# Kernel tuning notes

Measured on AMD Instinct MI355X. Metric: run time of the kernel, lower is better.

## Reference

```python
import jax, jax.numpy as jnp
import numpy as np

EPS = 1e-5
BS, NA, NC, NL, NPTS, ED, NG = 1, 900, 6, 4, 13, 256, 8
GD = ED // NG
IMG_W, IMG_H = 704.0, 256.0
FMAP_HW = [(64, 176), (32, 88), (16, 44), (8, 22)]


def _ln(x, g, b):
    m = x.mean(-1, keepdims=True)
    v = ((x - m) ** 2).mean(-1, keepdims=True)
    return (x - m) / jnp.sqrt(v + EPS) * g + b


def _grid_sample(img, grid):
    # img: [N,C,H,W]; grid: [N,P,Q,2] in [-1,1]; bilinear, zeros padding, align_corners=False
    N, C, H, W = img.shape
    gx = jnp.clip((grid[..., 0] + 1.0) * (W * 0.5) - 0.5, -1e4, 1e4)
    gy = jnp.clip((grid[..., 1] + 1.0) * (H * 0.5) - 0.5, -1e4, 1e4)
    x0 = jnp.floor(gx); y0 = jnp.floor(gy)
    wx1 = gx - x0; wy1 = gy - y0; wx0 = 1.0 - wx1; wy0 = 1.0 - wy1
    x0i = x0.astype(jnp.int32); y0i = y0.astype(jnp.int32)
    flat = img.reshape(N, C, H * W)

    def corner(xi, yi, wgt):
        valid = (xi >= 0) & (xi < W) & (yi >= 0) & (yi < H)
        idx = (jnp.clip(yi, 0, H - 1) * W + jnp.clip(xi, 0, W - 1))
        g = jax.vmap(lambda f, i: f[:, i])(flat, idx.reshape(N, -1))  # [N,C,P*Q]
        g = g.reshape(N, C, idx.shape[1], idx.shape[2])
        return g * (wgt * valid)[:, None]

    return (corner(x0i, y0i, wx0 * wy0) + corner(x0i + 1, y0i, wx1 * wy0)
            + corner(x0i, y0i + 1, wx0 * wy1) + corner(x0i + 1, y0i + 1, wx1 * wy1))


def setup_inputs() -> dict:
    key = jax.random.key(0)
    ks = jax.random.split(key, 20)
    d = {}
    d['instance_feature'] = jax.random.normal(ks[0], (BS, NA, ED), jnp.float32)
    xyz = jax.random.normal(ks[1], (BS, NA, 3), jnp.float32) * 1.5
    size = jax.random.normal(ks[2], (BS, NA, 3), jnp.float32) * 0.3
    theta = jax.random.uniform(ks[3], (BS, NA, 1), jnp.float32) * (2.0 * np.pi)
    vel = jax.random.normal(ks[4], (BS, NA, 3), jnp.float32) * 0.1
    d['anchor'] = jnp.concatenate([xyz, size, jnp.sin(theta), jnp.cos(theta), vel], -1)
    d['anchor_embed'] = jax.random.normal(ks[5], (BS, NA, ED), jnp.float32)
    for i, (h, w) in enumerate(FMAP_HW):
        d[f'fmap{i}'] = jax.random.normal(ks[6 + i], (BS, NC, ED, h, w), jnp.float32)
    base = jnp.array([[80., 0., 0., 352.], [0., 80., 0., 128.],
                      [0., 0., 0., 1.], [0., 0., 0., 1.]], jnp.float32)
    proj = jnp.tile(base, (BS, NC, 1, 1))
    proj = proj.at[:, :, :2, :].add(jax.random.normal(ks[10], (BS, NC, 2, 4), jnp.float32) * 2.0)
    d['projection_mat'] = proj
    d['image_wh'] = jnp.broadcast_to(jnp.array([IMG_W, IMG_H], jnp.float32), (BS, NC, 2))
    d['fix_scale'] = jnp.array([[0, 0, 0], [0.45, 0, 0], [-0.45, 0, 0], [0, 0.45, 0],
                                [0, -0.45, 0], [0, 0, 0.45], [0, 0, -0.45]], jnp.float32)

    def w(k, shape):
        return jax.random.normal(k, shape, jnp.float32) * 0.02

    d['lfc_w'] = w(ks[11], (ED, 6 * 3)); d['lfc_b'] = jnp.zeros((18,), jnp.float32)
    d['cam_w1'] = w(ks[12], (12, ED)); d['cam_b1'] = jnp.zeros((ED,), jnp.float32)
    d['cam_g1'] = jnp.ones((ED,), jnp.float32); d['cam_be1'] = jnp.zeros((ED,), jnp.float32)
    d['cam_w2'] = w(ks[13], (ED, ED)); d['cam_b2'] = jnp.zeros((ED,), jnp.float32)
    d['cam_g2'] = jnp.ones((ED,), jnp.float32); d['cam_be2'] = jnp.zeros((ED,), jnp.float32)
    d['wfc_w'] = w(ks[14], (ED, NG * NL * NPTS)); d['wfc_b'] = jnp.zeros((NG * NL * NPTS,), jnp.float32)
    d['op_w'] = w(ks[15], (ED, ED)); d['op_b'] = jnp.zeros((ED,), jnp.float32)
    return d


def reference(instance_feature, anchor, anchor_embed, fmap0, fmap1, fmap2, fmap3,
              projection_mat, image_wh, fix_scale, lfc_w, lfc_b,
              cam_w1, cam_b1, cam_g1, cam_be1, cam_w2, cam_b2, cam_g2, cam_be2,
              wfc_w, wfc_b, op_w, op_b):
    bs, na = instance_feature.shape[:2]
    # ---- keypoint generation ----
    size = jnp.exp(anchor[..., None, 3:6])                       # [bs,na,1,3]
    kp = fix_scale * size                                        # [bs,na,7,3]
    ls = jax.nn.sigmoid(instance_feature @ lfc_w + lfc_b).reshape(bs, na, -1, 3) - 0.5
    kp = jnp.concatenate([kp, ls * size], axis=-2)               # [bs,na,NPTS,3]
    sin, cos = anchor[..., 6:7], anchor[..., 7:8]                # [bs,na,1]
    kx, ky, kz = kp[..., 0], kp[..., 1], kp[..., 2]
    key_points = jnp.stack([cos * kx - sin * ky, sin * kx + cos * ky, kz], -1) \
                 + anchor[..., None, 0:3]                        # [bs,na,NPTS,3]
    # ---- per-cam/level/point group weights ----
    feat = instance_feature + anchor_embed
    cam_in = projection_mat[:, :, :3].reshape(bs, NC, 12)
    h = jax.nn.relu(cam_in @ cam_w1 + cam_b1); h = _ln(h, cam_g1, cam_be1)
    h = jax.nn.relu(h @ cam_w2 + cam_b2); cam_embed = _ln(h, cam_g2, cam_be2)
    f = feat[:, :, None] + cam_embed[:, None]                    # [bs,na,NC,ED]
    wts = (f @ wfc_w + wfc_b).reshape(bs, na, NC * NL * NPTS, NG)
    wts = jax.nn.softmax(wts, axis=-2).reshape(bs, na, NC, NL, NPTS, NG)
    # ---- multi-cam projection + bilinear sampling ----
    pts = jnp.concatenate([key_points, jnp.ones_like(key_points[..., :1])], -1)
    p2d = jnp.einsum('bcij,banj->bcani', projection_mat, pts)    # [bs,NC,na,NPTS,4]
    p2d = p2d[..., :2] / jnp.maximum(p2d[..., 2:3], 1e-5)
    p2d = p2d / image_wh[:, :, None, None]
    grid = (p2d * 2.0 - 1.0).reshape(bs * NC, na, NPTS, 2)
    feats = jnp.stack([_grid_sample(fm.reshape(bs * NC, ED, fm.shape[-2], fm.shape[-1]), grid)
                       for fm in (fmap0, fmap1, fmap2, fmap3)], axis=1)  # [bs*NC,NL,ED,na,NPTS]
    feats = feats.reshape(bs, NC, NL, ED, na, NPTS).transpose(0, 4, 1, 2, 5, 3)  # [bs,na,NC,NL,NPTS,ED]
    # ---- group-weighted fusion over cams & levels, then sum over points ----
    fg = feats.reshape(bs, na, NC, NL, NPTS, NG, GD)
    fused = jnp.einsum('bnclpg,bnclpgd->bnpgd', wts, fg).reshape(bs, na, NPTS, ED)
    fused = fused.sum(axis=2)                                    # [bs,na,ED]
    out = fused @ op_w + op_b
    return jnp.concatenate([out, instance_feature], axis=-1)     # [bs,na,2*ED]
```

## Files before the change

kernel.cpp:

```cpp
#include <hip/hip_runtime.h>
#include <stdint.h>

#define NA 900
#define NC 6
#define NL 4
#define NPTS 13
#define ED 256
#define NG 8
#define LNEPS 1e-5f
#define NTRANS 1416
#define NCOPY 672
#define NSAMP 312
#define LGS 313

struct PIn { const void* p[24]; };

__device__ __forceinline__ float b2f(unsigned short u){
  union { uint32_t i; float f; } v; v.i = ((uint32_t)u)<<16; return v.f;
}
__device__ __forceinline__ unsigned short f2b(float f){
  union { float f; uint32_t i; } v; v.f = f;
  uint32_t r = v.i + 0x7FFFu + ((v.i>>16)&1u);
  return (unsigned short)(r>>16);
}
#define BLO(u) __uint_as_float((u)<<16)
#define BHI(u) __uint_as_float((u)&0xffff0000u)

__device__ __forceinline__ float ldx(const void* p, int i, bool bf){
  return bf ? b2f(((const unsigned short*)p)[i]) : ((const float*)p)[i];
}

__device__ __forceinline__ bool sniff_bf(const unsigned short* __restrict__ u16){
  int lane = threadIdx.x & 63;
  unsigned short u = u16[2*lane];
  int e = (u>>7)&0xFF;
  int sane = (e>=110 && e<=135) ? 1 : 0;
  #pragma unroll
  for (int m=32;m;m>>=1) sane += __shfl_xor(sane, m);
  return sane >= 48;
}

__device__ __forceinline__ void blockReduce2(float& a, float& b, float* lds){
  #pragma unroll
  for (int m=32;m;m>>=1){ a += __shfl_xor(a,m); b += __shfl_xor(b,m); }
  int w = threadIdx.x>>6;
  if ((threadIdx.x&63)==0){ lds[w]=a; lds[w+4]=b; }
  __syncthreads();
  a = lds[0]+lds[1]+lds[2]+lds[3];
  b = lds[4]+lds[5]+lds[6]+lds[7];
  __syncthreads();
}

__global__ __launch_bounds__(256) void k_init(PIn in,
                                              unsigned short* __restrict__ wfcw_h,
                                              unsigned short* __restrict__ opw_h,
                                              float* __restrict__ Bc){
  const bool bf = sniff_bf((const unsigned short*)in.p[0]);
  const int tid = threadIdx.x;
  int b = blockIdx.x;

  __shared__ float h[ED];
  __shared__ float cE[ED];
  __shared__ float red8[8];
  __shared__ float part[4][64];

  if (b < NCOPY){
    int idx = b*256 + tid;
    if (idx < 106496){
      wfcw_h[idx] = bf ? ((const unsigned short*)in.p[20])[idx]
                       : f2b(((const float*)in.p[20])[idx]);
    } else {
      int j = idx - 106496;
      opw_h[j] = bf ? ((const unsigned short*)in.p[22])[j]
                    : f2b(((const float*)in.p[22])[j]);
    }
    return;
  }
  b -= NCOPY;
  {
    const void* proj = in.p[7];
    const void* w1 = in.p[12]; const void* b1 = in.p[13];
    const void* g1 = in.p[14]; const void* be1 = in.p[15];
    const void* w2 = in.p[16]; const void* b2 = in.p[17];
    const void* g2 = in.p[18]; const void* be2 = in.p[19];
    const void* wfcw = in.p[20]; const void* wfcb = in.p[21];
    const int c = b/7, colt = b - (b/7)*7;
    float ci[12];
    #pragma unroll
    for (int i=0;i<12;i++) ci[i] = ldx(proj, c*16+i, bf);
    float acc = ldx(b1, tid, bf);
    #pragma unroll
    for (int k=0;k<12;k++) acc += ci[k]*ldx(w1, k*ED+tid, bf);
    float x = fmaxf(acc, 0.f);
    float s=x, q=x*x;
    blockReduce2(s,q,red8);
    float mean = s*(1.f/ED), var = q*(1.f/ED)-mean*mean;
    h[tid] = (x-mean)*rsqrtf(var+LNEPS)*ldx(g1,tid,bf) + ldx(be1,tid,bf);
    __syncthreads();
    acc = ldx(b2, tid, bf);
    #pragma unroll 8
    for (int k=0;k<ED;k++) acc += h[k]*ldx(w2, k*ED+tid, bf);
    x = fmaxf(acc,0.f);
    s=x; q=x*x;
    blockReduce2(s,q,red8);
    mean = s*(1.f/ED); var = q*(1.f/ED)-mean*mean;
    cE[tid] = (x-mean)*rsqrtf(var+LNEPS)*ldx(g2,tid,bf) + ldx(be2,tid,bf);
    __syncthreads();
    const int kc = tid>>6, colL = tid&63, col = colt*64+colL;
    float a = 0.f;
    if (col < 416){
      #pragma unroll 8
      for (int k=0;k<64;k++) a += cE[kc*64+k]*ldx(wfcw, (kc*64+k)*416+col, bf);
    }
    part[kc][colL] = a;
    __syncthreads();
    if (kc==0 && col<416)
      Bc[c*416+col] = part[0][colL]+part[1][colL]+part[2][colL]+part[3][colL] + ldx(wfcb,col,bf);
  }
}

__global__ __launch_bounds__(256) void k_work(PIn in,
                                              unsigned short* __restrict__ tf,
                                              const unsigned short* __restrict__ wfcw_h,
                                              const float* __restrict__ Bc,
                                              uint4* __restrict__ gdesc, int* __restrict__ mcnt,
                                              void* __restrict__ outv){
  const bool bf = sniff_bf((const unsigned short*)in.p[0]);
  const int tid = threadIdx.x;
  int b = blockIdx.x;

  __shared__ unsigned short TT[2][64][64];
  __shared__ float ifs[ED];
  __shared__ float fe[ED];
  __shared__ float lg2[8*LGS];
  __shared__ float kp[13][3];
  __shared__ float sc[8];
  __shared__ float lsv[18];
  __shared__ int scnt;

  if (b < NTRANS){
    const int tiles[4] = {44,11,3,1};
    const int HWs[4]   = {11264,2816,704,176};
    const int TFO[4]   = {0,17301504,21626880,22708224};
    int l, local;
    if      (b < 1056){ l=0; local=b;      }
    else if (b < 1320){ l=1; local=b-1056; }
    else if (b < 1392){ l=2; local=b-1320; }
    else              { l=3; local=b-1392; }
    int pt = local % tiles[l]; int rest = local / tiles[l];
    int ct = rest & 3; int c = rest >> 2;
    const int HW = HWs[l];
    const int px0 = pt*256;
    const void* src = in.p[3+l];
    const int j8 = tid & 7;
    const int w8 = tid >> 3;

    uint4 v[2][4];
    float4 cf[2][4][2];
    if (bf){
      #pragma unroll
      for (int p=0;p<2;p++){
        int ch = ct*64 + p*32 + w8;
        size_t rowb = (size_t)(c*ED+ch)*HW;
        #pragma unroll
        for (int q=0;q<4;q++){
          int pxs = px0 + q*64 + j8*8;
          v[p][q] = (pxs < HW)
            ? *reinterpret_cast<const uint4*>((const unsigned short*)src + rowb + pxs)
            : make_uint4(0,0,0,0);
        }
      }
    } else {
      #pragma unroll
      for (int p=0;p<2;p++){
        int ch = ct*64 + p*32 + w8;
        size_t rowb = (size_t)(c*ED+ch)*HW;
        #pragma unroll
        for (int q=0;q<4;q++){
          int pxs = px0 + q*64 + j8*8;
          if (pxs < HW){
            cf[p][q][0] = *reinterpret_cast<const float4*>((const float*)src + rowb + pxs);
            cf[p][q][1] = *reinterpret_cast<const float4*>((const float*)src + rowb + pxs + 4);
          } else {
            cf[p][q][0] = make_float4(0.f,0.f,0.f,0.f);
            cf[p][q][1] = cf[p][q][0];
          }
        }
      }
    }
    for (int q=0;q<4;q++){
      if (px0 + q*64 >= HW) break;
      uint4 wv[2];
      if (bf){
        wv[0] = v[0][q]; wv[1] = v[1][q];
      } else {
        #pragma unroll
        for (int p=0;p<2;p++){
          wv[p].x = (uint32_t)f2b(cf[p][q][0].x) | ((uint32_t)f2b(cf[p][q][0].y)<<16);
          wv[p].y = (uint32_t)f2b(cf[p][q][0].z) | ((uint32_t)f2b(cf[p][q][0].w)<<16);
          wv[p].z = (uint32_t)f2b(cf[p][q][1].x) | ((uint32_t)f2b(cf[p][q][1].y)<<16);
          wv[p].w = (uint32_t)f2b(cf[p][q][1].z) | ((uint32_t)f2b(cf[p][q][1].w)<<16);
        }
      }
      const int buf = q & 1;
      #pragma unroll
      for (int p=0;p<2;p++){
        int r = p*32 + w8;
        int g8 = (j8 ^ (r>>3))<<3;
        *reinterpret_cast<uint4*>(&TT[buf][r][g8]) = wv[p];
      }
      __syncthreads();
      #pragma unroll
      for (int p=0;p<2;p++){
        int pxl = p*32 + w8;
        int px  = px0 + q*64 + pxl;
        int colq = (((pxl>>3) ^ j8)<<3) | (pxl & 7);
        int rb = j8*8;
        unsigned short t0 = TT[buf][rb+0][colq], t1 = TT[buf][rb+1][colq];
        unsigned short t2 = TT[buf][rb+2][colq], t3 = TT[buf][rb+3][colq];
        unsigned short t4 = TT[buf][rb+4][colq], t5 = TT[buf][rb+5][colq];
        unsigned short t6 = TT[buf][rb+6][colq], t7 = TT[buf][rb+7][colq];
        uint4 o;
        o.x = (uint32_t)t0 | ((uint32_t)t1<<16);
        o.y = (uint32_t)t2 | ((uint32_t)t3<<16);
        o.z = (uint32_t)t4 | ((uint32_t)t5<<16);
        o.w = (uint32_t)t6 | ((uint32_t)t7<<16);
        if (px < HW)
          *reinterpret_cast<uint4*>(tf + TFO[l] + (size_t)c*HW*ED + (size_t)px*ED + ct*64 + j8*8) = o;
      }
    }
    return;
  }
  const int n = b - NTRANS;
  const void* p_inst = in.p[0];
  const void* p_anc  = in.p[1];
  const void* p_ae   = in.p[2];
  const void* p_proj = in.p[7];
  const void* p_imwh = in.p[8];
  const void* p_fixs = in.p[9];
  const void* p_lw   = in.p[10];
  const void* p_lb   = in.p[11];

  {
    if (tid==0) scnt = 0;
    float iv = ldx(p_inst, n*ED+tid, bf);
    ifs[tid] = iv;
    fe[tid]  = iv + ldx(p_ae, n*ED+tid, bf);
    if (bf) ((unsigned short*)outv)[n*512+256+tid] = f2b(iv);
    else    ((float*)outv)[n*512+256+tid]          = iv;
    if (tid >= 256-8){
      int t = tid - (256-8);
      if (t < 3)       sc[t] = ldx(p_anc, n*11+t, bf);
      else if (t == 3) sc[3] = ldx(p_anc, n*11+6, bf);
      else if (t == 4) sc[4] = ldx(p_anc, n*11+7, bf);
      else             sc[t] = __expf(ldx(p_anc, n*11+t-2, bf));
    }
  }
  __syncthreads();
  if (tid < 144){
    int d = tid>>3, j = tid&7;
    float a = 0.f;
    #pragma unroll 8
    for (int k=j*32;k<j*32+32;k++) a += ifs[k]*ldx(p_lw, k*18+d, bf);
    a += __shfl_xor(a,1); a += __shfl_xor(a,2); a += __shfl_xor(a,4);
    if (j==0){
      a += ldx(p_lb, d, bf);
      lsv[d] = 1.f/(1.f+__expf(-a)) - 0.5f;
    }
  }
  __syncthreads();
  if (tid < 13){
    float kx,ky,kz;
    if (tid < 7){
      kx = ldx(p_fixs, tid*3+0, bf)*sc[5];
      ky = ldx(p_fixs, tid*3+1, bf)*sc[6];
      kz = ldx(p_fixs, tid*3+2, bf)*sc[7];
    } else {
      int j = tid-7;
      kx = lsv[j*3+0]*sc[5]; ky = lsv[j*3+1]*sc[6]; kz = lsv[j*3+2]*sc[7];
    }
    kp[tid][0] = sc[4]*kx - sc[3]*ky + sc[0];
    kp[tid][1] = sc[3]*kx + sc[4]*ky + sc[1];
    kp[tid][2] = kz + sc[2];
  }
  {
    int col2 = (tid < 160) ? tid+256 : 415;
    float a0 = 0.f, a1 = 0.f;
    #pragma unroll 4
    for (int k=0;k<ED;k++){
      float fv = fe[k];
      a0 += fv*b2f(wfcw_h[k*416+tid]);
      a1 += fv*b2f(wfcw_h[k*416+col2]);
    }
    const int g = tid & 7, rr = tid >> 3;
    const int g2 = col2 & 7, rr2 = col2 >> 3;
    #pragma unroll
    for (int c=0;c<NC;c++){
      lg2[g*LGS + c*52 + rr] = a0 + Bc[c*416+tid];
      if (tid < 160) lg2[g2*LGS + c*52 + rr2] = a1 + Bc[c*416+col2];
    }
  }
  __syncthreads();
  {
    const int g = tid>>5, j = tid&31;
    float v[10]; float mx = -1e30f;
    #pragma unroll
    for (int i=0;i<10;i++){
      int e = j + 32*i;
      float val = -1e30f;
      if (e < NSAMP){ val = lg2[g*LGS + e]; mx = fmaxf(mx, val); }
      v[i] = val;
    }
    #pragma unroll
    for (int mk=16;mk;mk>>=1) mx = fmaxf(mx, __shfl_xor(mx, mk, 32));
    float sum = 0.f;
    #pragma unroll
    for (int i=0;i<10;i++){
      if (j + 32*i < NSAMP){ float ex = __expf(v[i]-mx); v[i] = ex; sum += ex; }
    }
    #pragma unroll
    for (int mk=16;mk;mk>>=1) sum += __shfl_xor(sum, mk, 32);
    float inv = 1.f/sum;
    #pragma unroll
    for (int i=0;i<10;i++){
      int e = j + 32*i;
      if (e < NSAMP) lg2[g*LGS + e] = v[i]*inv;
    }
  }
  __syncthreads();
  #pragma unroll
  for (int pass=0;pass<2;pass++){
    int s = tid + pass*256;
    if (s < NSAMP){
      int c = s/52, rr = s - c*52;
      int l = rr/13, p = rr - l*13;
      float m[12];
      #pragma unroll
      for (int i=0;i<12;i++) m[i] = ldx(p_proj, c*16+i, bf);
      float X=kp[p][0], Y=kp[p][1], Z=kp[p][2];
      float x = m[0]*X + m[1]*Y + m[2]*Z  + m[3];
      float y = m[4]*X + m[5]*Y + m[6]*Z  + m[7];
      float z = m[8]*X + m[9]*Y + m[10]*Z + m[11];
      float d = fmaxf(z, 1e-5f);
      float px = x/(d*ldx(p_imwh, c*2+0, bf)), py = y/(d*ldx(p_imwh, c*2+1, bf));
      const int W = 176>>l, H = 64>>l;
      const int TFO[4] = {0,17301504,21626880,22708224};
      float gx = fminf(fmaxf(px*(float)W - 0.5f, -10000.f), 10000.f);
      float gy = fminf(fmaxf(py*(float)H - 0.5f, -10000.f), 10000.f);
      float xf = floorf(gx), yf = floorf(gy);
      int x0 = (int)xf, y0 = (int)yf;
      float wx1 = gx-xf, wy1 = gy-yf;
      float wx0 = 1.f-wx1, wy0 = 1.f-wy1;
      bool vx0 = (x0>=0)&&(x0<W),   vx1 = (x0+1>=0)&&(x0+1<W);
      bool vy0 = (y0>=0)&&(y0<H),   vy1 = (y0+1>=0)&&(y0+1<H);
      float w00 = (vx0&&vy0) ? wx0*wy0 : 0.f;
      float w10 = (vx1&&vy0) ? wx1*wy0 : 0.f;
      float w01 = (vx0&&vy1) ? wx0*wy1 : 0.f;
      float w11 = (vx1&&vy1) ? wx1*wy1 : 0.f;
      if (w00+w10+w01+w11 != 0.f){
        int cx0 = min(max(x0,0),W-1), cx1 = min(max(x0+1,0),W-1);
        int cy0 = min(max(y0,0),H-1), cy1 = min(max(y0+1,0),H-1);
        uint32_t cam = (uint32_t)TFO[l] + (uint32_t)(c*H*W)*ED;
        uint4 bi, wv;
        bi.x = cam + (uint32_t)(cy0*W+cx0)*ED;
        bi.y = cam + (uint32_t)(cy0*W+cx1)*ED;
        bi.z = cam + (uint32_t)(cy1*W+cx0)*ED;
        bi.w = cam + (uint32_t)(cy1*W+cx1)*ED;
        wv.x = __float_as_uint(w00); wv.y = __float_as_uint(w10);
        wv.z = __float_as_uint(w01); wv.w = __float_as_uint(w11);
        float4 wa = make_float4(lg2[0*LGS+s], lg2[1*LGS+s], lg2[2*LGS+s], lg2[3*LGS+s]);
        float4 wb = make_float4(lg2[4*LGS+s], lg2[5*LGS+s], lg2[6*LGS+s], lg2[7*LGS+s]);
        int slot = atomicAdd(&scnt, 1);
        uint4* dst = gdesc + (size_t)(n*NSAMP + slot)*4;
        dst[0] = bi;
        dst[1] = wv;
        dst[2] = *reinterpret_cast<uint4*>(&wa);
        dst[3] = *reinterpret_cast<uint4*>(&wb);
      }
    }
  }
  __syncthreads();
  if (tid==0) mcnt[n] = scnt;
}

__global__ __launch_bounds__(512, 4) void k_gather(
    const unsigned short* __restrict__ tf,
    const unsigned short* __restrict__ opw_h, const uint4* __restrict__ gdesc,
    const int* __restrict__ mcnt, const void* __restrict__ rawinst,
    const void* __restrict__ opb, void* __restrict__ outv){
  const int n = blockIdx.x, tid = threadIdx.x;
  const bool bf = sniff_bf((const unsigned short*)rawinst);

  __shared__ uint4 ldesc[NSAMP*4];
  __shared__ float red[8][ED+4];
  __shared__ float fu[ED];

  const int m = mcnt[n];
  {
    const uint4* src = gdesc + (size_t)n*NSAMP*4;
    for (int j=tid; j < m*4; j += 512) ldesc[j] = src[j];
  }
  __syncthreads();

  {
    const int strm = tid>>5, lane32 = tid&31;
    const int ch8 = lane32*8, gg = lane32>>2;
    float acc[8] = {0,0,0,0,0,0,0,0};
    int i = strm;
    for (; i + 16 < m; i += 32){
      uint4 biA = ldesc[i*4],      wfA = ldesc[i*4+1];
      uint4 biB = ldesc[(i+16)*4], wfB = ldesc[(i+16)*4+1];
      float wgA = reinterpret_cast<const float*>(&ldesc[i*4+2])[gg];
      float wgB = reinterpret_cast<const float*>(&ldesc[(i+16)*4+2])[gg];
      uint4 a00 = *reinterpret_cast<const uint4*>(tf + biA.x + ch8);
      uint4 a10 = *reinterpret_cast<const uint4*>(tf + biA.y + ch8);
      uint4 a01 = *reinterpret_cast<const uint4*>(tf + biA.z + ch8);
      uint4 a11 = *reinterpret_cast<const uint4*>(tf + biA.w + ch8);
      uint4 b00 = *reinterpret_cast<const uint4*>(tf + biB.x + ch8);
      uint4 b10 = *reinterpret_cast<const uint4*>(tf + biB.y + ch8);
      uint4 b01 = *reinterpret_cast<const uint4*>(tf + biB.z + ch8);
      uint4 b11 = *reinterpret_cast<const uint4*>(tf + biB.w + ch8);
      float pA00 = wgA*__uint_as_float(wfA.x), pA10 = wgA*__uint_as_float(wfA.y);
      float pA01 = wgA*__uint_as_float(wfA.z), pA11 = wgA*__uint_as_float(wfA.w);
      float pB00 = wgB*__uint_as_float(wfB.x), pB10 = wgB*__uint_as_float(wfB.y);
      float pB01 = wgB*__uint_as_float(wfB.z), pB11 = wgB*__uint_as_float(wfB.w);
      acc[0] += pA00*BLO(a00.x)+pA10*BLO(a10.x)+pA01*BLO(a01.x)+pA11*BLO(a11.x)
              + pB00*BLO(b00.x)+pB10*BLO(b10.x)+pB01*BLO(b01.x)+pB11*BLO(b11.x);
      acc[1] += pA00*BHI(a00.x)+pA10*BHI(a10.x)+pA01*BHI(a01.x)+pA11*BHI(a11.x)
              + pB00*BHI(b00.x)+pB10*BHI(b10.x)+pB01*BHI(b01.x)+pB11*BHI(b11.x);
      acc[2] += pA00*BLO(a00.y)+pA10*BLO(a10.y)+pA01*BLO(a01.y)+pA11*BLO(a11.y)
              + pB00*BLO(b00.y)+pB10*BLO(b10.y)+pB01*BLO(b01.y)+pB11*BLO(b11.y);
      acc[3] += pA00*BHI(a00.y)+pA10*BHI(a10.y)+pA01*BHI(a01.y)+pA11*BHI(a11.y)
              + pB00*BHI(b00.y)+pB10*BHI(b10.y)+pB01*BHI(b01.y)+pB11*BHI(b11.y);
      acc[4] += pA00*BLO(a00.z)+pA10*BLO(a10.z)+pA01*BLO(a01.z)+pA11*BLO(a11.z)
              + pB00*BLO(b00.z)+pB10*BLO(b10.z)+pB01*BLO(b01.z)+pB11*BLO(b11.z);
      acc[5] += pA00*BHI(a00.z)+pA10*BHI(a10.z)+pA01*BHI(a01.z)+pA11*BHI(a11.z)
              + pB00*BHI(b00.z)+pB10*BHI(b10.z)+pB01*BHI(b01.z)+pB11*BHI(b11.z);
      acc[6] += pA00*BLO(a00.w)+pA10*BLO(a10.w)+pA01*BLO(a01.w)+pA11*BLO(a11.w)
              + pB00*BLO(b00.w)+pB10*BLO(b10.w)+pB01*BLO(b01.w)+pB11*BLO(b11.w);
      acc[7] += pA00*BHI(a00.w)+pA10*BHI(a10.w)+pA01*BHI(a01.w)+pA11*BHI(a11.w)
              + pB00*BHI(b00.w)+pB10*BHI(b10.w)+pB01*BHI(b01.w)+pB11*BHI(b11.w);
    }
    for (; i < m; i += 16){
      uint4 bi = ldesc[i*4], wf = ldesc[i*4+1];
      float wg = reinterpret_cast<const float*>(&ldesc[i*4+2])[gg];
      uint4 q00 = *reinterpret_cast<const uint4*>(tf + bi.x + ch8);
      uint4 q10 = *reinterpret_cast<const uint4*>(tf + bi.y + ch8);
      uint4 q01 = *reinterpret_cast<const uint4*>(tf + bi.z + ch8);
      uint4 q11 = *reinterpret_cast<const uint4*>(tf + bi.w + ch8);
      float p00 = wg*__uint_as_float(wf.x), p10 = wg*__uint_as_float(wf.y);
      float p01 = wg*__uint_as_float(wf.z), p11 = wg*__uint_as_float(wf.w);
      acc[0] += p00*BLO(q00.x)+p10*BLO(q10.x)+p01*BLO(q01.x)+p11*BLO(q11.x);
      acc[1] += p00*BHI(q00.x)+p10*BHI(q10.x)+p01*BHI(q01.x)+p11*BHI(q11.x);
      acc[2] += p00*BLO(q00.y)+p10*BLO(q10.y)+p01*BLO(q01.y)+p11*BLO(q11.y);
      acc[3] += p00*BHI(q00.y)+p10*BHI(q10.y)+p01*BHI(q01.y)+p11*BHI(q11.y);
      acc[4] += p00*BLO(q00.z)+p10*BLO(q10.z)+p01*BLO(q01.z)+p11*BLO(q11.z);
      acc[5] += p00*BHI(q00.z)+p10*BHI(q10.z)+p01*BHI(q01.z)+p11*BHI(q11.z);
      acc[6] += p00*BLO(q00.w)+p10*BLO(q10.w)+p01*BLO(q01.w)+p11*BLO(q11.w);
      acc[7] += p00*BHI(q00.w)+p10*BHI(q10.w)+p01*BHI(q01.w)+p11*BHI(q11.w);
    }
    #pragma unroll
    for (int j=0;j<8;j++) acc[j] += __shfl_xor(acc[j], 32);
    const int w = tid>>6;
    if ((tid&63) < 32){
      *reinterpret_cast<float4*>(&red[w][ch8])   = make_float4(acc[0],acc[1],acc[2],acc[3]);
      *reinterpret_cast<float4*>(&red[w][ch8+4]) = make_float4(acc[4],acc[5],acc[6],acc[7]);
    }
  }
  __syncthreads();
  if (tid < 256){
    float r = 0.f;
    #pragma unroll
    for (int i=0;i<8;i++) r += red[i][tid];
    fu[tid] = r;
  }
  __syncthreads();
  {
    const int col = tid & 255, half = tid >> 8;
    const int k0 = half*128;
    float a = 0.f;
    #pragma unroll 8
    for (int k=k0;k<k0+128;k++) a += fu[k]*b2f(opw_h[k*ED+col]);
    red[half][col] = a;
  }
  __syncthreads();
  if (tid < 256){
    float v = ldx(opb, tid, bf) + red[0][tid] + red[1][tid];
    if (bf) ((unsigned short*)outv)[n*512+tid] = f2b(v);
    else    ((float*)outv)[n*512+tid]          = v;
  }
}

extern "C" void kernel_launch(void* const* d_in, const int* in_sizes, int n_in,
                              void* d_out, int out_size, void* d_ws, size_t ws_size,
                              hipStream_t stream){
  char* ws = (char*)d_ws;
  size_t off = 0;
  auto alloc = [&](size_t bytes)->char*{
    char* p = ws + off; off += (bytes + 63) & ~size_t(63); return p;
  };
  unsigned short* tf = (unsigned short*)alloc((size_t)22978560*2);
  unsigned short* wfcw_h = (unsigned short*)alloc((size_t)106496*2);
  unsigned short* opw_h  = (unsigned short*)alloc((size_t)65536*2);
  float* Bc     = (float*)alloc((size_t)NC*416*4);
  uint4* gdesc  = (uint4*)alloc((size_t)NA*NSAMP*64);
  int*   mcnt   = (int*)alloc((size_t)NA*4);

  PIn in;
  for (int i=0;i<24;i++) in.p[i] = d_in[i];

  k_init<<<NCOPY + 42, 256, 0, stream>>>(in, wfcw_h, opw_h, Bc);
  k_work<<<NTRANS + NA, 256, 0, stream>>>(in, tf, wfcw_h, Bc, gdesc, mcnt, d_out);
  k_gather<<<NA, 512, 0, stream>>>(tf, opw_h, gdesc, mcnt, d_in[0], d_in[23], d_out);
}
```

Before: 260.9 us.

## Stream fp32 feature-map transpose tiles via async global-to-LDS double buffering

```diff
diff --git a/kernel.cpp b/kernel.cpp
--- a/kernel.cpp
+++ b/kernel.cpp
@@ -28,6 +28,12 @@
 
 __device__ __forceinline__ float ldx(const void* p, int i, bool bf){
   return bf ? b2f(((const unsigned short*)p)[i]) : ((const float*)p)[i];
+}
+
+__device__ __forceinline__ void gload_lds16(const void* g, void* l){
+  __builtin_amdgcn_global_load_lds(
+      (const __attribute__((address_space(1))) void*)g,
+      (__attribute__((address_space(3))) void*)l, 16, 0, 0);
 }
 
 __device__ __forceinline__ bool sniff_bf(const unsigned short* __restrict__ u16){
@@ -129,14 +135,7 @@
   const int tid = threadIdx.x;
   int b = blockIdx.x;
 
-  __shared__ unsigned short TT[2][64][64];
-  __shared__ float ifs[ED];
-  __shared__ float fe[ED];
-  __shared__ float lg2[8*LGS];
-  __shared__ float kp[13][3];
-  __shared__ float sc[8];
-  __shared__ float lsv[18];
-  __shared__ int scnt;
+  __shared__ __align__(16) char smem[32768];
 
   if (b < NTRANS){
     const int tiles[4] = {44,11,3,1};
@@ -155,9 +154,66 @@
     const int j8 = tid & 7;
     const int w8 = tid >> 3;
 
-    uint4 v[2][4];
-    float4 cf[2][4][2];
-    if (bf){
+    int nq = 4;
+    while (nq > 1 && px0 + (nq-1)*64 >= HW) nq--;
+
+    if (!bf){
+      float* TTf = (float*)smem;
+      const int wv = tid >> 6;
+      const int ln = tid & 63;
+      const int rq = ln >> 4;
+      const int g  = ln & 15;
+
+      auto issueph = [&](int q){
+        const int pxq = px0 + q*64;
+        float* dst0 = TTf + (q&1)*4096;
+        #pragma unroll
+        for (int i=0;i<4;i++){
+          int r   = wv*16 + i*4 + rq;
+          int swz = (r>>3) & 7;
+          int px  = pxq + 4*(g ^ swz);
+          if (px + 4 > HW) px = HW - 4;
+          const float* gsrc = (const float*)src + (size_t)(c*ED + ct*64 + r)*HW + px;
+          gload_lds16(gsrc, (void*)(dst0 + (wv*16 + i*4)*64));
+        }
+      };
+
+      issueph(0);
+      for (int q=0; q<nq; q++){
+        if (q+1 < nq){
+          issueph(q+1);
+          asm volatile("s_waitcnt vmcnt(4)" ::: "memory");
+        } else {
+          asm volatile("s_waitcnt vmcnt(0)" ::: "memory");
+        }
+        __builtin_amdgcn_s_barrier();
+        const float* T = TTf + (q&1)*4096;
+        #pragma unroll
+        for (int p=0;p<2;p++){
+          int pxl = p*32 + w8;
+          int px  = px0 + q*64 + pxl;
+          int s   = 4*((pxl>>2) ^ j8) + (pxl&3);
+          if (px < HW){
+            unsigned short u[8];
+            #pragma unroll
+            for (int k=0;k<8;k++)
+              u[k] = f2b(T[(j8*8+k)*64 + s]);
+            uint4 o;
+            o.x = (uint32_t)u[0] | ((uint32_t)u[1]<<16);
+            o.y = (uint32_t)u[2] | ((uint32_t)u[3]<<16);
+            o.z = (uint32_t)u[4] | ((uint32_t)u[5]<<16);
+            o.w = (uint32_t)u[6] | ((uint32_t)u[7]<<16);
+            *reinterpret_cast<uint4*>(tf + TFO[l] + (size_t)c*HW*ED + (size_t)px*ED + ct*64 + j8*8) = o;
+          }
+        }
+        __builtin_amdgcn_s_barrier();
+      }
+      return;
+    }
+    {
+      typedef unsigned short u16tile[64][64];
+      u16tile* TT = (u16tile*)smem;
+      uint4 v[2][4];
       #pragma unroll
       for (int p=0;p<2;p++){
         int ch = ct*64 + p*32 + w8;
@@ -170,68 +226,46 @@
             : make_uint4(0,0,0,0);
         }
       }
-    } else {
-      #pragma unroll
-      for (int p=0;p<2;p++){
-        int ch = ct*64 + p*32 + w8;
-        size_t rowb = (size_t)(c*ED+ch)*HW;
+      for (int q=0;q<nq;q++){
+        const int buf = q & 1;
         #pragma unroll
-        for (int q=0;q<4;q++){
-          int pxs = px0 + q*64 + j8*8;
-          if (pxs < HW){
-            cf[p][q][0] = *reinterpret_cast<const float4*>((const float*)src + rowb + pxs);
-            cf[p][q][1] = *reinterpret_cast<const float4*>((const float*)src + rowb + pxs + 4);
-          } else {
-            cf[p][q][0] = make_float4(0.f,0.f,0.f,0.f);
-            cf[p][q][1] = cf[p][q][0];
-          }
+        for (int p=0;p<2;p++){
+          int r = p*32 + w8;
+          int g8 = (j8 ^ (r>>3))<<3;
+          *reinterpret_cast<uint4*>(&TT[buf][r][g8]) = v[p][q];
+        }
+        __syncthreads();
+        #pragma unroll
+        for (int p=0;p<2;p++){
+          int pxl = p*32 + w8;
+          int px  = px0 + q*64 + pxl;
+          int colq = (((pxl>>3) ^ j8)<<3) | (pxl & 7);
+          int rb = j8*8;
+          unsigned short t0 = TT[buf][rb+0][colq], t1 = TT[buf][rb+1][colq];
+          unsigned short t2 = TT[buf][rb+2][colq], t3 = TT[buf][rb+3][colq];
+          unsigned short t4 = TT[buf][rb+4][colq], t5 = TT[buf][rb+5][colq];
+          unsigned short t6 = TT[buf][rb+6][colq], t7 = TT[buf][rb+7][colq];
+          uint4 o;
+          o.x = (uint32_t)t0 | ((uint32_t)t1<<16);
+          o.y = (uint32_t)t2 | ((uint32_t)t3<<16);
+          o.z = (uint32_t)t4 | ((uint32_t)t5<<16);
+          o.w = (uint32_t)t6 | ((uint32_t)t7<<16);
+          if (px < HW)
+            *reinterpret_cast<uint4*>(tf + TFO[l] + (size_t)c*HW*ED + (size_t)px*ED + ct*64 + j8*8) = o;
         }
       }
-    }
-    for (int q=0;q<4;q++){
-      if (px0 + q*64 >= HW) break;
-      uint4 wv[2];
-      if (bf){
-        wv[0] = v[0][q]; wv[1] = v[1][q];
-      } else {
-        #pragma unroll
-        for (int p=0;p<2;p++){
-          wv[p].x = (uint32_t)f2b(cf[p][q][0].x) | ((uint32_t)f2b(cf[p][q][0].y)<<16);
-          wv[p].y = (uint32_t)f2b(cf[p][q][0].z) | ((uint32_t)f2b(cf[p][q][0].w)<<16);
-          wv[p].z = (uint32_t)f2b(cf[p][q][1].x) | ((uint32_t)f2b(cf[p][q][1].y)<<16);
-          wv[p].w = (uint32_t)f2b(cf[p][q][1].z) | ((uint32_t)f2b(cf[p][q][1].w)<<16);
-        }
-      }
-      const int buf = q & 1;
-      #pragma unroll
-      for (int p=0;p<2;p++){
-        int r = p*32 + w8;
-        int g8 = (j8 ^ (r>>3))<<3;
-        *reinterpret_cast<uint4*>(&TT[buf][r][g8]) = wv[p];
-      }
-      __syncthreads();
-      #pragma unroll
-      for (int p=0;p<2;p++){
-        int pxl = p*32 + w8;
-        int px  = px0 + q*64 + pxl;
-        int colq = (((pxl>>3) ^ j8)<<3) | (pxl & 7);
-        int rb = j8*8;
-        unsigned short t0 = TT[buf][rb+0][colq], t1 = TT[buf][rb+1][colq];
-        unsigned short t2 = TT[buf][rb+2][colq], t3 = TT[buf][rb+3][colq];
-        unsigned short t4 = TT[buf][rb+4][colq], t5 = TT[buf][rb+5][colq];
-        unsigned short t6 = TT[buf][rb+6][colq], t7 = TT[buf][rb+7][colq];
-        uint4 o;
-        o.x = (uint32_t)t0 | ((uint32_t)t1<<16);
-        o.y = (uint32_t)t2 | ((uint32_t)t3<<16);
-        o.z = (uint32_t)t4 | ((uint32_t)t5<<16);
-        o.w = (uint32_t)t6 | ((uint32_t)t7<<16);
-        if (px < HW)
-          *reinterpret_cast<uint4*>(tf + TFO[l] + (size_t)c*HW*ED + (size_t)px*ED + ct*64 + j8*8) = o;
-      }
-    }
-    return;
+      return;
+    }
   }
   const int n = b - NTRANS;
+  float* ifs = (float*)(smem);
+  float* fe  = (float*)(smem + 1024);
+  float* lg2 = (float*)(smem + 2048);
+  float (*kp)[3] = (float (*)[3])(smem + 12160);
+  float* sc  = (float*)(smem + 12352);
+  float* lsv = (float*)(smem + 12416);
+  int*   scnt= (int*)(smem + 12544);
+
   const void* p_inst = in.p[0];
   const void* p_anc  = in.p[1];
   const void* p_ae   = in.p[2];
@@ -242,7 +276,7 @@
   const void* p_lb   = in.p[11];
 
   {
-    if (tid==0) scnt = 0;
+    if (tid==0) *scnt = 0;
     float iv = ldx(p_inst, n*ED+tid, bf);
     ifs[tid] = iv;
     fe[tid]  = iv + ldx(p_ae, n*ED+tid, bf);
@@ -370,7 +404,7 @@
         wv.z = __float_as_uint(w01); wv.w = __float_as_uint(w11);
         float4 wa = make_float4(lg2[0*LGS+s], lg2[1*LGS+s], lg2[2*LGS+s], lg2[3*LGS+s]);
         float4 wb = make_float4(lg2[4*LGS+s], lg2[5*LGS+s], lg2[6*LGS+s], lg2[7*LGS+s]);
-        int slot = atomicAdd(&scnt, 1);
+        int slot = atomicAdd(scnt, 1);
         uint4* dst = gdesc + (size_t)(n*NSAMP + slot)*4;
         dst[0] = bi;
         dst[1] = wv;
@@ -380,7 +414,7 @@
     }
   }
   __syncthreads();
-  if (tid==0) mcnt[n] = scnt;
+  if (tid==0) mcnt[n] = *scnt;
 }
 
 __global__ __launch_bounds__(512, 4) void k_gather(
```

Result: no change. 259.2 us (-0.7%).
